# Performance work log

Hardware: AMD Instinct MI355X
Metric: run time of the kernel (lower is better)

Reference implementation:

```python
import jax, jax.numpy as jnp
import numpy as np

LOGZERO = -1e10
BLANK, EOS = 0, 2
B, T, O = 8, 500, 10000
W = 8          # beam width -> n_bh = B*W hypotheses
SNUM = 200     # CTC pre-scoring label count


def setup_inputs() -> dict:
    key = jax.random.key(0)
    k1, k2, k3, k4, k5, k6 = jax.random.split(key, 6)
    n_bh = B * W
    # label log-posteriors (B, T, O)
    x = jax.nn.log_softmax(jax.random.normal(k1, (B, T, O), jnp.float32), axis=-1)
    xlens = jax.random.randint(k2, (B,), T // 2, T + 1).astype(jnp.int32)
    last_ids = jax.random.randint(k3, (n_bh,), 0, O).astype(jnp.int32)
    # unique scoring ids per hypothesis (pre-selected labels)
    scoring_ids = jax.vmap(lambda k: jax.random.permutation(k, O)[:SNUM])(
        jax.random.split(k4, n_bh)).astype(jnp.int32)
    r_prev = jax.random.normal(k5, (T, 2, n_bh), jnp.float32) - 5.0
    s_prev = jax.random.normal(k6, (n_bh, O), jnp.float32) * 0.1
    return dict(x=x, r_prev=r_prev, s_prev=s_prev, xlens=xlens,
                last_ids=last_ids, scoring_ids=scoring_ids, output_length=10)


def _forward(x, r_prev, s_prev, xlens, last_ids, scoring_ids, output_length):
    n_bh = last_ids.shape[0]
    n_hyps = n_bh // B
    snum = scoring_ids.shape[1]

    # ---- __init__: mask frames t >= xlens[b]: logzero everywhere, 0 at blank ----
    tmask = jnp.arange(T)[None, :] >= xlens[:, None]                    # (B,T)
    x = jnp.where(tmask[:, :, None], LOGZERO, x)
    x = x.at[:, :, BLANK].set(jnp.where(tmask, 0.0, x[:, :, BLANK]))
    xn = jnp.transpose(x, (1, 0, 2))                                    # (T,B,O)
    xb = jnp.broadcast_to(xn[:, :, BLANK][:, :, None], xn.shape)        # (T,B,O)
    xs = jnp.stack([xn, xb])                                            # (2,T,B,O)
    end_frames = xlens - 1

    b_of_hyp = jnp.arange(n_bh) // n_hyps                               # (n_bh,)
    # scoring_idmap: (n_bh, O), position of each label in scoring list, -1 if absent
    idmap = jnp.full((n_bh, O), -1, jnp.int32).at[
        jnp.arange(n_bh)[:, None], scoring_ids].set(
        jnp.broadcast_to(jnp.arange(snum, dtype=jnp.int32)[None, :], (n_bh, snum)))
    # gather scored labels: (2,T,n_bh,snum)
    x_ = xs[:, :, b_of_hyp[:, None], scoring_ids]

    r_sum = jax.scipy.special.logsumexp(r_prev, axis=1)                 # (T,n_bh)
    pos = idmap[jnp.arange(n_bh), last_ids]                             # (n_bh,)
    hit = (jnp.arange(snum)[None, :] == pos[:, None]) & (pos[:, None] >= 0)
    # log_phi: r_sum, except r_prev[:,1] where next label == last label
    log_phi = jnp.where(hit[None], r_prev[:, 1, :, None], r_sum[:, :, None])  # (T,n_bh,snum)

    start = max(int(output_length), 1)

    r0 = jnp.full((2, n_bh, snum), LOGZERO, x.dtype)
    if output_length == 0:
        r0 = r0.at[0].set(x_[0, 0])

    def step(rp, inp):
        phi_tm1, x_t = inp                                              # (n_bh,snum),(2,n_bh,snum)
        rn = jnp.logaddexp(rp[0], phi_tm1) + x_t[0]
        rb = jnp.logaddexp(rp[0], rp[1]) + x_t[1]
        rt = jnp.stack([rn, rb])
        return rt, rt

    _, r_scan = jax.lax.scan(step, r0,
                             (log_phi[start - 1:T - 1],
                              jnp.moveaxis(x_[:, start:T], 1, 0)))       # (T-start,2,n_bh,snum)
    r_pre = jnp.full((start, 2, n_bh, snum), LOGZERO, x.dtype)
    if output_length == 0:
        r_pre = r_pre.at[0, 0].set(x_[0, 0])
    r = jnp.concatenate([r_pre, r_scan], axis=0)                        # (T,2,n_bh,snum)

    # log_psi over scored labels
    log_phi_x = jnp.concatenate([log_phi[:1], log_phi[:-1]], axis=0) + x_[0]   # (T,n_bh,snum)
    psi_stack = jnp.concatenate([log_phi_x[start:T], r[start - 1, 0][None]], axis=0)
    log_psi_ = jax.scipy.special.logsumexp(psi_stack, axis=0)           # (n_bh,snum)

    log_psi = jnp.full((n_bh, O), LOGZERO, x.dtype).at[
        jnp.arange(n_bh)[:, None], scoring_ids].set(log_psi_)
    eos_score = r_sum[end_frames[b_of_hyp], jnp.arange(n_bh)]
    log_psi = log_psi.at[:, EOS].set(eos_score)
    log_psi = log_psi.at[:, BLANK].set(LOGZERO)
    return log_psi - s_prev                                             # (n_bh, O)


def reference(x, r_prev, s_prev, xlens, last_ids, scoring_ids, output_length):
    return _forward(x, r_prev, s_prev, xlens, last_ids, scoring_ids, output_length)
```

## Files before the change

kernel.cpp:

```cpp
#include <hip/hip_runtime.h>

#define LOGZERO -10000000000.0f

constexpr int Bc    = 8;
constexpr int Tc    = 500;
constexpr int Oc    = 10000;
constexpr int NBH   = 64;
constexpr int NHYP  = 8;
constexpr int SNUM  = 200;
constexpr int BLANK = 0;
constexpr int EOSID = 2;

constexpr int TC     = 4;
constexpr int NCHUNK = (Tc + TC - 1) / TC;
constexpr int NSCORE = Bc * NCHUNK;
constexpr int NP     = 7;
constexpr int NV4    = Oc / 4;
constexpr int FULLI  = NV4 / 256;
constexpr int REMT   = NV4 - FULLI * 256;

__device__ __forceinline__ float logaddexp_f(float a, float b) {
    float m = fmaxf(a, b);
    return m + log1pf(expf(-fabsf(a - b)));
}

__global__ __launch_bounds__(256) void ctc_main_kernel(
    const float* __restrict__ x,
    const float* __restrict__ r_prev,
    const float* __restrict__ s_prev,
    const int*   __restrict__ xlens,
    const int*   __restrict__ last_ids,
    const int*   __restrict__ scoring_ids,
    const int*   __restrict__ olen_p,
    float*       __restrict__ acc_out,
    float*       __restrict__ out)
{
    const int blk = blockIdx.x;
    const int tid = threadIdx.x;

    if (blk >= NSCORE) {
        const int h = blk - NSCORE;
        const int b = h >> 3;
        const int end = xlens[b] - 1;
        const float r0 = r_prev[(size_t)end * (2 * NBH) + h];
        const float r1 = r_prev[(size_t)end * (2 * NBH) + NBH + h];
        const float eos = logaddexp_f(r0, r1);

        const float4* sp4  = (const float4*)(s_prev + (size_t)h * Oc);
        float4*       out4 = (float4*)(out + (size_t)h * Oc);
        for (int idx = tid; idx < NV4; idx += 256) {
            float4 s = sp4[idx];
            int o = idx * 4;
            float4 v;
            v.x = ((o + 0 == EOSID) ? eos : LOGZERO) - s.x;
            v.y = ((o + 1 == EOSID) ? eos : LOGZERO) - s.y;
            v.z = ((o + 2 == EOSID) ? eos : LOGZERO) - s.z;
            v.w = ((o + 3 == EOSID) ? eos : LOGZERO) - s.w;
            out4[idx] = v;
        }
        return;
    }

    const int c  = blk >> 3;
    const int b  = blk & 7;
    const int t0 = c * TC;

    const int ol    = olen_p[0];
    const int start = (ol > 1) ? ol : 1;
    const int tlo   = (ol == 0) ? 0 : start;
    int xlen = xlens[b];
    if (xlen > Tc) xlen = Tc;
    const int lo = (t0 > tlo) ? t0 : tlo;
    const int hi = ((t0 + TC) < xlen) ? (t0 + TC) : xlen;
    if (lo >= hi) return;
    const int nt = hi - lo;

    __shared__ __align__(16) float xrow[Oc];
    __shared__ float pnoL[TC][NHYP];
    __shared__ float phitL[TC][NHYP];

    if (tid < nt * NHYP) {
        const int ti = tid >> 3;
        const int j  = tid & 7;
        const int t  = lo + ti;
        if (t == 0) {
            pnoL[ti][j]  = 0.0f;
            phitL[ti][j] = 0.0f;
        } else {
            const int h = b * NHYP + j;
            const float r0 = r_prev[(size_t)(t - 1) * (2 * NBH) + h];
            const float r1 = r_prev[(size_t)(t - 1) * (2 * NBH) + NBH + h];
            phitL[ti][j] = r1;
            pnoL[ti][j]  = logaddexp_f(r0, r1);
        }
    }

    int   sid[NP];
    int   jj[NP];
    bool  hit[NP];
    float acc[NP];
#pragma unroll
    for (int i = 0; i < NP; ++i) {
        acc[i] = 0.0f;
        int p = tid + i * 256;
        if (p < NHYP * SNUM) {
            int j = p / SNUM;
            int k = p - j * SNUM;
            int h = b * NHYP + j;
            int s = scoring_ids[h * SNUM + k];
            sid[i] = s;
            jj[i]  = j;
            hit[i] = (s == last_ids[h]);
        } else {
            sid[i] = 0; jj[i] = 0; hit[i] = false;
        }
    }

    for (int t = lo, ti = 0; t < hi; ++t, ++ti) {
        const float4* row4 = (const float4*)(x + (size_t)(b * Tc + t) * Oc);
        float4* x4 = (float4*)xrow;
        float4 buf[FULLI + 1];
#pragma unroll
        for (int i = 0; i < FULLI; ++i) buf[i] = row4[tid + i * 256];
        if (tid < REMT) buf[FULLI] = row4[tid + FULLI * 256];
#pragma unroll
        for (int i = 0; i < FULLI; ++i) x4[tid + i * 256] = buf[i];
        if (tid < REMT) x4[tid + FULLI * 256] = buf[FULLI];
        __syncthreads();

#pragma unroll
        for (int i = 0; i < NP; ++i) {
            int p = tid + i * 256;
            if (p < NHYP * SNUM) {
                float ph = hit[i] ? phitL[ti][jj[i]] : pnoL[ti][jj[i]];
                acc[i] += expf(ph + xrow[sid[i]]);
            }
        }
        __syncthreads();
    }

#pragma unroll
    for (int i = 0; i < NP; ++i) {
        int p = tid + i * 256;
        if (p < NHYP * SNUM && acc[i] != 0.0f) {
            int j = jj[i];
            int k = p - j * SNUM;
            int h = b * NHYP + j;
            atomicAdd(&acc_out[h * SNUM + k], acc[i]);
        }
    }
}

__global__ __launch_bounds__(256) void ctc_scatter_kernel(
    const float* __restrict__ s_prev,
    const int*   __restrict__ scoring_ids,
    const float* __restrict__ acc_in,
    float*       __restrict__ out)
{
    const int h   = blockIdx.x;
    const int tid = threadIdx.x;
    if (tid < SNUM) {
        int o = scoring_ids[h * SNUM + tid];
        if (o != BLANK && o != EOSID) {
            float sum = acc_in[h * SNUM + tid];
            sum = fmaxf(sum, 1e-37f);
            float psi = logf(sum);
            out[(size_t)h * Oc + o] = psi - s_prev[(size_t)h * Oc + o];
        }
    }
}

extern "C" void kernel_launch(void* const* d_in, const int* in_sizes, int n_in,
                              void* d_out, int out_size, void* d_ws, size_t ws_size,
                              hipStream_t stream) {
    const float* x           = (const float*)d_in[0];
    const float* r_prev      = (const float*)d_in[1];
    const float* s_prev      = (const float*)d_in[2];
    const int*   xlens       = (const int*)d_in[3];
    const int*   last_ids    = (const int*)d_in[4];
    const int*   scoring_ids = (const int*)d_in[5];
    const int*   olen        = (const int*)d_in[6];
    float* out = (float*)d_out;
    float* acc = (float*)d_ws;

    hipMemsetAsync(acc, 0, NBH * SNUM * sizeof(float), stream);
    ctc_main_kernel<<<NSCORE + NBH, 256, 0, stream>>>(
        x, r_prev, s_prev, xlens, last_ids, scoring_ids, olen, acc, out);
    ctc_scatter_kernel<<<NBH, 256, 0, stream>>>(
        s_prev, scoring_ids, acc, out);
}
```

Measured before the change: 258.6 us.

## Replace global atomics and memset with per-chunk partials reduced in scatter kernel

```diff
diff --git a/kernel.cpp b/kernel.cpp
--- a/kernel.cpp
+++ b/kernel.cpp
@@ -14,17 +14,16 @@
 constexpr int TC     = 4;
 constexpr int NCHUNK = (Tc + TC - 1) / TC;
 constexpr int NSCORE = Bc * NCHUNK;
+constexpr int NPAIR  = NHYP * SNUM;
 constexpr int NP     = 7;
 constexpr int NV4    = Oc / 4;
-constexpr int FULLI  = NV4 / 256;
-constexpr int REMT   = NV4 - FULLI * 256;
 
 __device__ __forceinline__ float logaddexp_f(float a, float b) {
     float m = fmaxf(a, b);
     return m + log1pf(expf(-fabsf(a - b)));
 }
 
-__global__ __launch_bounds__(256) void ctc_main_kernel(
+__global__ __launch_bounds__(256, 4) void ctc_main_kernel(
     const float* __restrict__ x,
     const float* __restrict__ r_prev,
     const float* __restrict__ s_prev,
@@ -32,7 +31,7 @@
     const int*   __restrict__ last_ids,
     const int*   __restrict__ scoring_ids,
     const int*   __restrict__ olen_p,
-    float*       __restrict__ acc_out,
+    float*       __restrict__ part,
     float*       __restrict__ out)
 {
     const int blk = blockIdx.x;
@@ -65,6 +64,8 @@
     const int b  = blk & 7;
     const int t0 = c * TC;
 
+    float* __restrict__ myPart = part + ((size_t)c * NBH + b * NHYP) * SNUM;
+
     const int ol    = olen_p[0];
     const int start = (ol > 1) ? ol : 1;
     const int tlo   = (ol == 0) ? 0 : start;
@@ -72,68 +73,64 @@
     if (xlen > Tc) xlen = Tc;
     const int lo = (t0 > tlo) ? t0 : tlo;
     const int hi = ((t0 + TC) < xlen) ? (t0 + TC) : xlen;
-    if (lo >= hi) return;
+    if (lo >= hi) {
+        for (int p = tid; p < NPAIR; p += 256) myPart[p] = 0.0f;
+        return;
+    }
     const int nt = hi - lo;
 
     __shared__ __align__(16) float xrow[Oc];
-    __shared__ float pnoL[TC][NHYP];
-    __shared__ float phitL[TC][NHYP];
+    __shared__ float phiL[2 * TC * NHYP];
 
     if (tid < nt * NHYP) {
         const int ti = tid >> 3;
         const int j  = tid & 7;
         const int t  = lo + ti;
         if (t == 0) {
-            pnoL[ti][j]  = 0.0f;
-            phitL[ti][j] = 0.0f;
+            phiL[ti * NHYP + j]              = 0.0f;
+            phiL[TC * NHYP + ti * NHYP + j]  = 0.0f;
         } else {
             const int h = b * NHYP + j;
             const float r0 = r_prev[(size_t)(t - 1) * (2 * NBH) + h];
             const float r1 = r_prev[(size_t)(t - 1) * (2 * NBH) + NBH + h];
-            phitL[ti][j] = r1;
-            pnoL[ti][j]  = logaddexp_f(r0, r1);
+            phiL[ti * NHYP + j]             = logaddexp_f(r0, r1);
+            phiL[TC * NHYP + ti * NHYP + j] = r1;
         }
     }
 
     int   sid[NP];
-    int   jj[NP];
-    bool  hit[NP];
+    int   hoff[NP];
     float acc[NP];
 #pragma unroll
     for (int i = 0; i < NP; ++i) {
         acc[i] = 0.0f;
         int p = tid + i * 256;
-        if (p < NHYP * SNUM) {
+        if (p < NPAIR) {
             int j = p / SNUM;
             int k = p - j * SNUM;
             int h = b * NHYP + j;
             int s = scoring_ids[h * SNUM + k];
-            sid[i] = s;
-            jj[i]  = j;
-            hit[i] = (s == last_ids[h]);
+            sid[i]  = s;
+            hoff[i] = ((s == last_ids[h]) ? TC * NHYP : 0) + j;
         } else {
-            sid[i] = 0; jj[i] = 0; hit[i] = false;
+            sid[i] = 0; hoff[i] = 0;
         }
     }
 
     for (int t = lo, ti = 0; t < hi; ++t, ++ti) {
         const float4* row4 = (const float4*)(x + (size_t)(b * Tc + t) * Oc);
         float4* x4 = (float4*)xrow;
-        float4 buf[FULLI + 1];
-#pragma unroll
-        for (int i = 0; i < FULLI; ++i) buf[i] = row4[tid + i * 256];
-        if (tid < REMT) buf[FULLI] = row4[tid + FULLI * 256];
-#pragma unroll
-        for (int i = 0; i < FULLI; ++i) x4[tid + i * 256] = buf[i];
-        if (tid < REMT) x4[tid + FULLI * 256] = buf[FULLI];
+        for (int idx = tid; idx < NV4; idx += 256) {
+            x4[idx] = row4[idx];
+        }
         __syncthreads();
 
+        const int tb = ti * NHYP;
 #pragma unroll
         for (int i = 0; i < NP; ++i) {
             int p = tid + i * 256;
-            if (p < NHYP * SNUM) {
-                float ph = hit[i] ? phitL[ti][jj[i]] : pnoL[ti][jj[i]];
-                acc[i] += expf(ph + xrow[sid[i]]);
+            if (p < NPAIR) {
+                acc[i] += expf(phiL[hoff[i] + tb] + xrow[sid[i]]);
             }
         }
         __syncthreads();
@@ -142,30 +139,29 @@
 #pragma unroll
     for (int i = 0; i < NP; ++i) {
         int p = tid + i * 256;
-        if (p < NHYP * SNUM && acc[i] != 0.0f) {
-            int j = jj[i];
-            int k = p - j * SNUM;
-            int h = b * NHYP + j;
-            atomicAdd(&acc_out[h * SNUM + k], acc[i]);
-        }
+        if (p < NPAIR) myPart[p] = acc[i];
     }
 }
 
-__global__ __launch_bounds__(256) void ctc_scatter_kernel(
+__global__ __launch_bounds__(256) void ctc_reduce_scatter_kernel(
     const float* __restrict__ s_prev,
     const int*   __restrict__ scoring_ids,
-    const float* __restrict__ acc_in,
+    const float* __restrict__ part,
     float*       __restrict__ out)
 {
     const int h   = blockIdx.x;
     const int tid = threadIdx.x;
     if (tid < SNUM) {
+        float sum = 0.0f;
+        const float* p = part + (size_t)h * SNUM + tid;
+#pragma unroll 5
+        for (int c = 0; c < NCHUNK; ++c) {
+            sum += p[(size_t)c * NBH * SNUM];
+        }
         int o = scoring_ids[h * SNUM + tid];
         if (o != BLANK && o != EOSID) {
-            float sum = acc_in[h * SNUM + tid];
             sum = fmaxf(sum, 1e-37f);
-            float psi = logf(sum);
-            out[(size_t)h * Oc + o] = psi - s_prev[(size_t)h * Oc + o];
+            out[(size_t)h * Oc + o] = logf(sum) - s_prev[(size_t)h * Oc + o];
         }
     }
 }
@@ -180,12 +176,11 @@
     const int*   last_ids    = (const int*)d_in[4];
     const int*   scoring_ids = (const int*)d_in[5];
     const int*   olen        = (const int*)d_in[6];
-    float* out = (float*)d_out;
-    float* acc = (float*)d_ws;
+    float* out  = (float*)d_out;
+    float* part = (float*)d_ws;
 
-    hipMemsetAsync(acc, 0, NBH * SNUM * sizeof(float), stream);
     ctc_main_kernel<<<NSCORE + NBH, 256, 0, stream>>>(
-        x, r_prev, s_prev, xlens, last_ids, scoring_ids, olen, acc, out);
-    ctc_scatter_kernel<<<NBH, 256, 0, stream>>>(
-        s_prev, scoring_ids, acc, out);
+        x, r_prev, s_prev, xlens, last_ids, scoring_ids, olen, part, out);
+    ctc_reduce_scatter_kernel<<<NBH, 256, 0, stream>>>(
+        s_prev, scoring_ids, part, out);
 }
```

After: 242.5 us. 6.2% less time.
